# Kernel optimization log

Measured on AMD Instinct MI355X. Metric: run time of the kernel, lower is better.

## Reference

```python
import jax, jax.numpy as jnp
import numpy as np

RADIUS = 0.08          # fixed search radius (module init arg)
MAX_NEIGHBORS = 64     # pad cap; expected ~35 neighbors/query at this density


def setup_inputs() -> dict:
    key = jax.random.key(0)
    k1, k2 = jax.random.split(key)
    return {
        "inp_positions": jax.random.uniform(k1, (16384, 3), dtype=jnp.float32),
        "out_positions": jax.random.uniform(k2, (16384, 3), dtype=jnp.float32),
    }


def reference(inp_positions, out_positions):
    """Fixed-radius neighbor search.

    Returns (neighbors_index [M, MAX_NEIGHBORS] int32, padded with -1,
             neighbors_row_splits [M+1] int32) --- the padded/static-shape
    equivalent of the ragged CSR output of NeighborSearchReturn.
    """
    r2 = jnp.float32(RADIUS * RADIUS)
    # pairwise squared distances [M, N]
    diff = out_positions[:, None, :] - inp_positions[None, :, :]
    d2 = jnp.sum(diff * diff, axis=-1)
    within = d2 <= r2                                   # [M, N] bool
    counts = jnp.minimum(within.sum(axis=1), MAX_NEIGHBORS).astype(jnp.int32)
    # rank in-radius points first (nearest first); -inf for out-of-radius
    score = jnp.where(within, -d2, -jnp.inf)
    _, idx = jax.lax.top_k(score, MAX_NEIGHBORS)        # [M, K]
    valid = jnp.arange(MAX_NEIGHBORS, dtype=jnp.int32)[None, :] < counts[:, None]
    neighbors_index = jnp.where(valid, idx, -1).astype(jnp.int32)
    row_splits = jnp.concatenate(
        [jnp.zeros((1,), jnp.int32), jnp.cumsum(counts).astype(jnp.int32)]
    )
    return neighbors_index, row_splits
```

## Files before the change

### kernel.cpp

```cpp
#include <hip/hip_runtime.h>

#define MAXNB 64
#define CAP   128
#define GRID  12
#define NCELL (GRID * GRID * GRID)

__device__ __forceinline__ int cell_of(float x, float y, float z) {
  int cx = min(GRID - 1, max(0, (int)(x * (float)GRID)));
  int cy = min(GRID - 1, max(0, (int)(y * (float)GRID)));
  int cz = min(GRID - 1, max(0, (int)(z * (float)GRID)));
  return (cz * GRID + cy) * GRID + cx;
}

__global__ __launch_bounds__(256) void build_kernel(
    const float* __restrict__ inp, const float* __restrict__ qry,
    float4* __restrict__ ppack, float4* __restrict__ qpack,
    int* __restrict__ pcell, int* __restrict__ ppos,
    int* __restrict__ pcellcnt, int n, int m) {
  int i = blockIdx.x * 256 + threadIdx.x;
  if (i < n) {
    float x = inp[3 * i], y = inp[3 * i + 1], z = inp[3 * i + 2];
    ppack[i] = make_float4(x, y, z, 0.f);
    int c = cell_of(x, y, z);
    pcell[i] = c;
    ppos[i] = atomicAdd(&pcellcnt[c], 1);
  }
  if (i < m) {
    qpack[i] = make_float4(qry[3 * i], qry[3 * i + 1], qry[3 * i + 2], 0.f);
  }
}

__global__ __launch_bounds__(256) void cellscan_kernel(
    const int* __restrict__ pcnt, int* __restrict__ pstart) {
  __shared__ int part[256];
  int t = threadIdx.x;
  int base = t * 7;
  int v[7];
  int s = 0;
#pragma unroll
  for (int i = 0; i < 7; ++i) {
    int idx = base + i;
    int c = (idx < NCELL) ? pcnt[idx] : 0;
    v[i] = c;
    s += c;
  }
  part[t] = s;
  __syncthreads();
  for (int off = 1; off < 256; off <<= 1) {
    int vv = (t >= off) ? part[t - off] : 0;
    __syncthreads();
    part[t] += vv;
    __syncthreads();
  }
  int run = (t == 0) ? 0 : part[t - 1];
#pragma unroll
  for (int i = 0; i < 7; ++i) {
    int idx = base + i;
    if (idx <= NCELL) pstart[idx] = run;
    run += v[i];
  }
}

__global__ __launch_bounds__(256) void scatter_kernel(
    const float4* __restrict__ ppack, const int* __restrict__ pcell,
    const int* __restrict__ ppos, const int* __restrict__ pstart,
    float4* __restrict__ psorted, int n) {
  int i = blockIdx.x * 256 + threadIdx.x;
  if (i < n) {
    float4 p = ppack[i];
    p.w = __int_as_float(i);
    psorted[pstart[pcell[i]] + ppos[i]] = p;
  }
}

__global__ __launch_bounds__(256) void scanrank_kernel(
    const float4* __restrict__ psorted, const float4* __restrict__ qpack,
    const int* __restrict__ pstart, int* __restrict__ cnt,
    int* __restrict__ nbr) {
#pragma clang fp contract(off)
  const float R2 = (float)(0.08 * 0.08);
  const float RM = 0.0801f;
  __shared__ float sd2[4][CAP];
  __shared__ int sidx[4][CAP];
  __shared__ int souts[4][MAXNB];
  int w = threadIdx.x >> 6;
  int lane = threadIdx.x & 63;
  int q = blockIdx.x * 4 + w;
  float4 Q = qpack[q];

  int x0 = max(0, (int)floorf((Q.x - RM) * (float)GRID));
  int x1 = min(GRID - 1, (int)floorf((Q.x + RM) * (float)GRID));
  int y0 = max(0, (int)floorf((Q.y - RM) * (float)GRID));
  int y1 = min(GRID - 1, (int)floorf((Q.y + RM) * (float)GRID));
  int z0 = max(0, (int)floorf((Q.z - RM) * (float)GRID));
  int z1 = min(GRID - 1, (int)floorf((Q.z + RM) * (float)GRID));

  int nc = 0;
  for (int z = z0; z <= z1; ++z) {
    for (int y = y0; y <= y1; ++y) {
      int rowbase = (z * GRID + y) * GRID;
      int k0 = pstart[rowbase + x0];
      int k1 = pstart[rowbase + x1 + 1];
      for (int kb = k0; kb < k1; kb += 64) {
        int k = kb + lane;
        bool hit = false;
        float d2 = 0.f;
        int id = 0;
        if (k < k1) {
          float4 P = psorted[k];
          float dx = Q.x - P.x;
          float dy = Q.y - P.y;
          float dz = Q.z - P.z;
          d2 = dx * dx + dy * dy + dz * dz;
          id = __float_as_int(P.w);
          hit = d2 <= R2;
        }
        unsigned long long b = __ballot(hit);
        int pre = __builtin_amdgcn_mbcnt_hi(
            (unsigned)(b >> 32), __builtin_amdgcn_mbcnt_lo((unsigned)b, 0));
        int slot = nc + pre;
        if (hit && slot < CAP) {
          sd2[w][slot] = d2;
          sidx[w][slot] = id;
        }
        nc += __popcll(b);
      }
    }
  }

  if (lane == 0) cnt[q] = nc;
  souts[w][lane] = -1;
  __syncthreads();

  int ncc = nc < CAP ? nc : CAP;
  for (int c = lane; c < ncc; c += 64) {
    float myd = sd2[w][c];
    int myi = sidx[w][c];
    int rank = 0;
    for (int j = 0; j < ncc; ++j) {
      float dj = sd2[w][j];
      int ij = sidx[w][j];
      rank += (dj < myd) || (dj == myd && ij < myi);
    }
    if (rank < MAXNB) souts[w][rank] = myi;
  }
  __syncthreads();

  nbr[(size_t)q * MAXNB + lane] = souts[w][lane];
}

__global__ __launch_bounds__(256) void splits_kernel(
    const int* __restrict__ cnt, int* __restrict__ rs, int m) {
  __shared__ int part[256];
  int t = threadIdx.x;
  int per = m / 256;
  int base = t * per;
  const int4* c4 = (const int4*)(cnt + base);
  int s = 0;
#pragma unroll
  for (int i = 0; i < 16; ++i) {
    int4 v = c4[i];
    s += min(v.x, MAXNB) + min(v.y, MAXNB) + min(v.z, MAXNB) + min(v.w, MAXNB);
  }
  part[t] = s;
  __syncthreads();
  for (int off = 1; off < 256; off <<= 1) {
    int v = (t >= off) ? part[t - off] : 0;
    __syncthreads();
    part[t] += v;
    __syncthreads();
  }
  int run = (t == 0) ? 0 : part[t - 1];
  if (t == 0) rs[0] = 0;
#pragma unroll
  for (int i = 0; i < 16; ++i) {
    int4 v = c4[i];
    run += min(v.x, MAXNB); rs[base + 4 * i + 1] = run;
    run += min(v.y, MAXNB); rs[base + 4 * i + 2] = run;
    run += min(v.z, MAXNB); rs[base + 4 * i + 3] = run;
    run += min(v.w, MAXNB); rs[base + 4 * i + 4] = run;
  }
}

extern "C" void kernel_launch(void* const* d_in, const int* in_sizes, int n_in,
                              void* d_out, int out_size, void* d_ws, size_t ws_size,
                              hipStream_t stream) {
  const float* inp = (const float*)d_in[0];
  const float* qry = (const float*)d_in[1];
  int n = in_sizes[0] / 3;
  int m = in_sizes[1] / 3;

  char* ws = (char*)d_ws;
  size_t off = 0;
  float4* ppack   = (float4*)(ws + off); off += (size_t)n * 16;
  float4* qpack   = (float4*)(ws + off); off += (size_t)m * 16;
  float4* psorted = (float4*)(ws + off); off += (size_t)n * 16;
  int* pcell    = (int*)(ws + off); off += (size_t)n * 4;
  int* ppos     = (int*)(ws + off); off += (size_t)n * 4;
  int* cnt      = (int*)(ws + off); off += (size_t)m * 4;
  int* pcellcnt = (int*)(ws + off); off += (size_t)NCELL * 4;
  int* pstart   = (int*)(ws + off); off += (size_t)(NCELL + 1) * 4;

  int* nbr = (int*)d_out;
  int* rs = nbr + (size_t)m * MAXNB;

  hipMemsetAsync(pcellcnt, 0, (size_t)NCELL * 4, stream);

  int mx = n > m ? n : m;
  hipLaunchKernelGGL(build_kernel, dim3((mx + 255) / 256), dim3(256), 0, stream,
                     inp, qry, ppack, qpack, pcell, ppos, pcellcnt, n, m);
  hipLaunchKernelGGL(cellscan_kernel, dim3(1), dim3(256), 0, stream,
                     pcellcnt, pstart);
  hipLaunchKernelGGL(scatter_kernel, dim3((n + 255) / 256), dim3(256), 0, stream,
                     ppack, pcell, ppos, pstart, psorted, n);
  hipLaunchKernelGGL(scanrank_kernel, dim3(m / 4), dim3(256), 0, stream,
                     psorted, qpack, pstart, cnt, nbr);
  hipLaunchKernelGGL(splits_kernel, dim3(1), dim3(256), 0, stream, cnt, rs, m);
}
```

Baseline: 97.09 us.

## Flatten cell-row scan across wave, pack sort keys, drop ppack and syncs

The neighbor scan now gathers all cell rows into one flat range, up to nine rows via shared prefix offsets, so each 64-lane chunk can span row boundaries instead of leaving lanes idle on short rows. Distance and index are packed into one 64-bit key so the rank sort does a single compare per pair. The intermediate ppack buffer is removed: scatter reads the input positions directly. Block-wide __syncthreads are dropped because each wave only touches its own shared slice, which relies on wave-level execution order for the shared writes.

```diff
diff --git a/kernel.cpp b/kernel.cpp
--- a/kernel.cpp
+++ b/kernel.cpp
@@ -14,13 +14,11 @@
 
 __global__ __launch_bounds__(256) void build_kernel(
     const float* __restrict__ inp, const float* __restrict__ qry,
-    float4* __restrict__ ppack, float4* __restrict__ qpack,
-    int* __restrict__ pcell, int* __restrict__ ppos,
+    float4* __restrict__ qpack, int* __restrict__ pcell, int* __restrict__ ppos,
     int* __restrict__ pcellcnt, int n, int m) {
   int i = blockIdx.x * 256 + threadIdx.x;
   if (i < n) {
     float x = inp[3 * i], y = inp[3 * i + 1], z = inp[3 * i + 2];
-    ppack[i] = make_float4(x, y, z, 0.f);
     int c = cell_of(x, y, z);
     pcell[i] = c;
     ppos[i] = atomicAdd(&pcellcnt[c], 1);
@@ -62,13 +60,13 @@
 }
 
 __global__ __launch_bounds__(256) void scatter_kernel(
-    const float4* __restrict__ ppack, const int* __restrict__ pcell,
+    const float* __restrict__ inp, const int* __restrict__ pcell,
     const int* __restrict__ ppos, const int* __restrict__ pstart,
     float4* __restrict__ psorted, int n) {
   int i = blockIdx.x * 256 + threadIdx.x;
   if (i < n) {
-    float4 p = ppack[i];
-    p.w = __int_as_float(i);
+    float4 p = make_float4(inp[3 * i], inp[3 * i + 1], inp[3 * i + 2],
+                           __int_as_float(i));
     psorted[pstart[pcell[i]] + ppos[i]] = p;
   }
 }
@@ -80,8 +78,9 @@
 #pragma clang fp contract(off)
   const float R2 = (float)(0.08 * 0.08);
   const float RM = 0.0801f;
-  __shared__ float sd2[4][CAP];
-  __shared__ int sidx[4][CAP];
+  __shared__ unsigned long long skey[4][CAP];
+  __shared__ int srk0[4][10];
+  __shared__ int sracc[4][10];
   __shared__ int souts[4][MAXNB];
   int w = threadIdx.x >> 6;
   int lane = threadIdx.x & 63;
@@ -95,56 +94,61 @@
   int z0 = max(0, (int)floorf((Q.z - RM) * (float)GRID));
   int z1 = min(GRID - 1, (int)floorf((Q.z + RM) * (float)GRID));
 
-  int nc = 0;
+  int nr = 0, tot = 0;
   for (int z = z0; z <= z1; ++z) {
     for (int y = y0; y <= y1; ++y) {
-      int rowbase = (z * GRID + y) * GRID;
-      int k0 = pstart[rowbase + x0];
-      int k1 = pstart[rowbase + x1 + 1];
-      for (int kb = k0; kb < k1; kb += 64) {
-        int k = kb + lane;
-        bool hit = false;
-        float d2 = 0.f;
-        int id = 0;
-        if (k < k1) {
-          float4 P = psorted[k];
-          float dx = Q.x - P.x;
-          float dy = Q.y - P.y;
-          float dz = Q.z - P.z;
-          d2 = dx * dx + dy * dy + dz * dz;
-          id = __float_as_int(P.w);
-          hit = d2 <= R2;
-        }
-        unsigned long long b = __ballot(hit);
-        int pre = __builtin_amdgcn_mbcnt_hi(
-            (unsigned)(b >> 32), __builtin_amdgcn_mbcnt_lo((unsigned)b, 0));
-        int slot = nc + pre;
-        if (hit && slot < CAP) {
-          sd2[w][slot] = d2;
-          sidx[w][slot] = id;
-        }
-        nc += __popcll(b);
-      }
+      int rb = (z * GRID + y) * GRID;
+      int k0 = pstart[rb + x0];
+      int k1 = pstart[rb + x1 + 1];
+      if (lane == 0) { srk0[w][nr] = k0; sracc[w][nr] = tot; }
+      tot += k1 - k0;
+      ++nr;
     }
+  }
+
+  int nc = 0;
+  for (int tb = 0; tb < tot; tb += 64) {
+    int t = tb + lane;
+    bool hit = false;
+    float d2 = 0.f;
+    int id = 0;
+    if (t < tot) {
+      int r = 0;
+#pragma unroll
+      for (int s = 1; s < 9; ++s)
+        if (s < nr && t >= sracc[w][s]) r = s;
+      int k = srk0[w][r] + (t - sracc[w][r]);
+      float4 P = psorted[k];
+      float dx = Q.x - P.x;
+      float dy = Q.y - P.y;
+      float dz = Q.z - P.z;
+      d2 = dx * dx + dy * dy + dz * dz;
+      id = __float_as_int(P.w);
+      hit = d2 <= R2;
+    }
+    unsigned long long b = __ballot(hit);
+    int pre = __builtin_amdgcn_mbcnt_hi(
+        (unsigned)(b >> 32), __builtin_amdgcn_mbcnt_lo((unsigned)b, 0));
+    int slot = nc + pre;
+    if (hit && slot < CAP) {
+      skey[w][slot] =
+          ((unsigned long long)(unsigned)__float_as_int(d2) << 32) |
+          (unsigned)id;
+    }
+    nc += __popcll(b);
   }
 
   if (lane == 0) cnt[q] = nc;
   souts[w][lane] = -1;
-  __syncthreads();
 
   int ncc = nc < CAP ? nc : CAP;
   for (int c = lane; c < ncc; c += 64) {
-    float myd = sd2[w][c];
-    int myi = sidx[w][c];
+    unsigned long long mykey = skey[w][c];
     int rank = 0;
-    for (int j = 0; j < ncc; ++j) {
-      float dj = sd2[w][j];
-      int ij = sidx[w][j];
-      rank += (dj < myd) || (dj == myd && ij < myi);
-    }
-    if (rank < MAXNB) souts[w][rank] = myi;
-  }
-  __syncthreads();
+    for (int j = 0; j < ncc; ++j)
+      rank += (skey[w][j] < mykey);
+    if (rank < MAXNB) souts[w][rank] = (int)(unsigned)mykey;
+  }
 
   nbr[(size_t)q * MAXNB + lane] = souts[w][lane];
 }
@@ -192,7 +196,6 @@
 
   char* ws = (char*)d_ws;
   size_t off = 0;
-  float4* ppack   = (float4*)(ws + off); off += (size_t)n * 16;
   float4* qpack   = (float4*)(ws + off); off += (size_t)m * 16;
   float4* psorted = (float4*)(ws + off); off += (size_t)n * 16;
   int* pcell    = (int*)(ws + off); off += (size_t)n * 4;
@@ -208,11 +211,11 @@
 
   int mx = n > m ? n : m;
   hipLaunchKernelGGL(build_kernel, dim3((mx + 255) / 256), dim3(256), 0, stream,
-                     inp, qry, ppack, qpack, pcell, ppos, pcellcnt, n, m);
+                     inp, qry, qpack, pcell, ppos, pcellcnt, n, m);
   hipLaunchKernelGGL(cellscan_kernel, dim3(1), dim3(256), 0, stream,
                      pcellcnt, pstart);
   hipLaunchKernelGGL(scatter_kernel, dim3((n + 255) / 256), dim3(256), 0, stream,
-                     ppack, pcell, ppos, pstart, psorted, n);
+                     inp, pcell, ppos, pstart, psorted, n);
   hipLaunchKernelGGL(scanrank_kernel, dim3(m / 4), dim3(256), 0, stream,
                      psorted, qpack, pstart, cnt, nbr);
   hipLaunchKernelGGL(splits_kernel, dim3(1), dim3(256), 0, stream, cnt, rs, m);
```

Result: faster. 93.00 us (-4.2%).
